# Optimization experiments

Hardware: AMD Instinct MI355X
Metric: run time of the kernel (lower is better)

## Reference

```python
import jax, jax.numpy as jnp
import numpy as np

CUTOFF = 5.0           # module init kwarg
NSYS, NAT = 64, 1000   # 64 systems of 1000 atoms each
BOX = 21.544           # cubic box edge -> ~0.1 atoms/A^3 (water-like density)
MAX_PAIRS = 2_200_000


def setup_inputs() -> dict:
    key = jax.random.key(0)
    coords = jax.random.uniform(key, (NSYS * NAT, 3), dtype=jnp.float32) * BOX
    isys = jnp.repeat(jnp.arange(NSYS, dtype=jnp.int32), NAT)
    natoms = jnp.full((NSYS,), NAT, dtype=jnp.int32)
    return {"coordinates": coords, "isys": isys, "natoms": natoms}


def reference(coordinates, isys, natoms):
    # Fixed-capacity cutoff neighbor list (no PBC branch), faithful to
    # GraphGeneratorFixed: half-list (i<j, same system), squared distances d12,
    # compacted into a MAX_PAIRS buffer padded with padding_value=N, then
    # symmetrized by concatenation.
    nsys = natoms.shape[0]
    n = coordinates.shape[0]
    nat = n // nsys                      # equal-sized systems (static)
    padding_value = n
    cutoff2 = jnp.float32(CUTOFF * CUTOFF)

    x = coordinates.reshape(nsys, nat, 3)                 # [S, nat, 3]
    sq = jnp.sum(x * x, axis=-1)                          # [S, nat]
    gram = jnp.einsum('sid,sjd->sij', x, x)               # [S, nat, nat]
    d12 = sq[:, :, None] + sq[:, None, :] - 2.0 * gram    # squared distances

    triu = jnp.triu(jnp.ones((nat, nat), dtype=bool), k=1)  # i < j half-list
    mask = (d12 < cutoff2) & triu[None, :, :]             # [S, nat, nat]
    mflat = mask.reshape(-1)                              # [S*nat*nat]
    npairs = jnp.sum(mflat)

    # stream-compaction: position of each kept pair in the output buffer
    pos = jnp.cumsum(mflat.astype(jnp.int32)) - 1
    sel = jnp.where(mflat, pos, MAX_PAIRS)                # OOB -> dropped
    flat_idx = jnp.arange(nsys * nat * nat, dtype=jnp.int32)
    idx_buf = jnp.full((MAX_PAIRS,), -1, dtype=jnp.int32).at[sel].set(
        flat_idx, mode='drop')

    valid = idx_buf >= 0
    ib = jnp.maximum(idx_buf, 0)
    s = ib // (nat * nat)
    rem = ib % (nat * nat)
    i = rem // nat
    j = rem % nat
    src = jnp.where(valid, s * nat + i, padding_value)
    dst = jnp.where(valid, s * nat + j, padding_value)
    d12_sel = jnp.where(valid, d12.reshape(-1)[ib], cutoff2)

    # symmetrize (directed graph), as in the original
    edge_src = jnp.concatenate([src, dst])
    edge_dst = jnp.concatenate([dst, src])
    d12_out = jnp.concatenate([d12_sel, d12_sel])
    return edge_src, edge_dst, d12_out, npairs
```

## Files before the change

kernel.cpp:

```cpp
#include <hip/hip_runtime.h>

#define NSYS 64
#define NAT  1000
#define NTOT (NSYS * NAT)
#define MP   2200000
#define CUT2 25.0f
#define PADV 64000.0f
#define SCAN_BLOCKS 250
#define CAP  104
#define EB   512
#define LCN  1152

__device__ __forceinline__ float dist2f(float xi, float yi, float zi,
                                        float xj, float yj, float zj) {
    float dx = xi - xj, dy = yi - yj, dz = zi - zj;
    return fmaf(dz, dz, fmaf(dy, dy, dx * dx));
}

__global__ __launch_bounds__(1024) void k_eval(const float* __restrict__ coords,
                                               int* __restrict__ counts,
                                               uint2* __restrict__ qbuf) {
    __shared__ float4 lc[LCN];
    int s      = blockIdx.x >> 3;
    int stripe = blockIdx.x & 7;
    const float* cs = coords + s * (NAT * 3);
    for (int a = threadIdx.x; a < NAT; a += 1024)
        lc[a] = make_float4(cs[3 * a], cs[3 * a + 1], cs[3 * a + 2], 0.0f);
    __syncthreads();
    int w    = threadIdx.x >> 6;
    int lane = threadIdx.x & 63;
    int W    = stripe * 16 + w;
    unsigned long long lt = (1ull << lane) - 1ull;
    for (int r = W; r < NAT; r += 128) {
        float4 ci = lc[r];
        int grow = s * NAT + r;
        uint2* q = qbuf + (size_t)grow * CAP;
        int running = 0;
        for (int jb = r + 1; jb < NAT; jb += 128) {
            int j  = jb + lane;
            int j2 = j + 64;
            float4 c0 = lc[j];
            float4 c1 = lc[j2];
            float d0 = dist2f(ci.x, ci.y, ci.z, c0.x, c0.y, c0.z);
            float d1 = dist2f(ci.x, ci.y, ci.z, c1.x, c1.y, c1.z);
            bool k0 = (j  < NAT) && (d0 < CUT2);
            bool k1 = (j2 < NAT) && (d1 < CUT2);
            unsigned long long m0 = __ballot(k0);
            unsigned long long m1 = __ballot(k1);
            if (k0) {
                int rank = running + (int)__popcll(m0 & lt);
                if (rank < CAP)
                    q[rank] = make_uint2((unsigned)(j - r), __float_as_uint(d0));
            }
            int base1 = running + (int)__popcll(m0);
            if (k1) {
                int rank = base1 + (int)__popcll(m1 & lt);
                if (rank < CAP)
                    q[rank] = make_uint2((unsigned)(j2 - r), __float_as_uint(d1));
            }
            running = base1 + (int)__popcll(m1);
        }
        if (lane == 0) counts[grow] = running;
    }
}

__global__ void k_scan_a(const int* __restrict__ counts, int* __restrict__ offs,
                         int* __restrict__ bsum) {
    __shared__ int tmp[256];
    int t = threadIdx.x;
    int g = blockIdx.x * 256 + t;
    int v = counts[g];
    tmp[t] = v;
    __syncthreads();
    for (int off = 1; off < 256; off <<= 1) {
        int u = (t >= off) ? tmp[t - off] : 0;
        __syncthreads();
        tmp[t] += u;
        __syncthreads();
    }
    offs[g] = tmp[t] - v;
    if (t == 255) bsum[blockIdx.x] = tmp[255];
}

__global__ __launch_bounds__(1024) void k_emitpad(const int* __restrict__ counts,
                                                  const int* __restrict__ offs,
                                                  const int* __restrict__ bsum,
                                                  const uint2* __restrict__ qbuf,
                                                  float* __restrict__ out) {
    __shared__ int bpre[256];
    __shared__ int stot;
    int t = threadIdx.x;
    int v = 0;
    if (t < 256) {
        v = (t < SCAN_BLOCKS) ? bsum[t] : 0;
        bpre[t] = v;
    }
    __syncthreads();
    for (int off = 1; off < 256; off <<= 1) {
        int u = 0;
        if (t < 256 && t >= off) u = bpre[t - off];
        __syncthreads();
        if (t < 256) bpre[t] += u;
        __syncthreads();
    }
    int incl = (t < 256) ? bpre[t] : 0;
    __syncthreads();
    if (t < 256) bpre[t] = incl - v;
    if (t == 255) stot = incl;
    __syncthreads();

    int wv   = t >> 6;
    int lane = t & 63;
    int GW   = blockIdx.x * 16 + wv;
    for (int r = GW; r < NTOT; r += EB * 16) {
        int off = offs[r] + bpre[r >> 8];
        int cnt = counts[r];
        if (cnt > CAP) cnt = CAP;
        const uint2* q = qbuf + (size_t)r * CAP;
        float fs = (float)r;
        for (int l = lane; l < cnt; l += 64) {
            uint2 e = q[l];
            int pos = off + l;
            if (pos < MP) {
                float fd = (float)(r + (int)e.x);
                float d2 = __uint_as_float(e.y);
                out[pos]          = fs;
                out[MP + pos]     = fd;
                out[2 * MP + pos] = fd;
                out[3 * MP + pos] = fs;
                out[4 * MP + pos] = d2;
                out[5 * MP + pos] = d2;
            }
        }
    }

    int total = stot;
    if (blockIdx.x == 0 && t == 0) out[6 * MP] = (float)total;
    int valid = total < MP ? total : MP;
    const int NQ = MP / 4;
    for (int q4 = blockIdx.x * 1024 + t; q4 < NQ; q4 += EB * 1024) {
        int k4 = q4 * 4;
        if (k4 + 4 <= valid) continue;
        if (k4 >= valid) {
            float4 vp = {PADV, PADV, PADV, PADV};
            float4 vc = {CUT2, CUT2, CUT2, CUT2};
            *(float4*)(out + k4)          = vp;
            *(float4*)(out + MP + k4)     = vp;
            *(float4*)(out + 2 * MP + k4) = vp;
            *(float4*)(out + 3 * MP + k4) = vp;
            *(float4*)(out + 4 * MP + k4) = vc;
            *(float4*)(out + 5 * MP + k4) = vc;
        } else {
#pragma unroll
            for (int e = 0; e < 4; e++) {
                int k = k4 + e;
                if (k >= valid && k < MP) {
                    out[k]          = PADV;
                    out[MP + k]     = PADV;
                    out[2 * MP + k] = PADV;
                    out[3 * MP + k] = PADV;
                    out[4 * MP + k] = CUT2;
                    out[5 * MP + k] = CUT2;
                }
            }
        }
    }
}

extern "C" void kernel_launch(void* const* d_in, const int* in_sizes, int n_in,
                              void* d_out, int out_size, void* d_ws, size_t ws_size,
                              hipStream_t stream) {
    const float* coords = (const float*)d_in[0];
    float* out = (float*)d_out;

    int*   counts = (int*)d_ws;
    int*   offs   = counts + NTOT;
    int*   bsum   = offs + NTOT;
    uint2* qbuf   = (uint2*)(bsum + 256);

    k_eval<<<EB, 1024, 0, stream>>>(coords, counts, qbuf);
    k_scan_a<<<SCAN_BLOCKS, 256, 0, stream>>>(counts, offs, bsum);
    k_emitpad<<<EB, 1024, 0, stream>>>(counts, offs, bsum, qbuf, out);
}
```

Before: 113.4 us.

## Make emit output-position-centric with binary search; zigzag row balancing in eval

The emit kernel is reorganised so each thread owns four consecutive output slots. A block-level binary search over the row prefix offsets, followed by a shared-memory search per thread, finds the source row for each slot. Every output column is then written with one coalesced float4 store that covers valid pairs and padding alike, replacing the row-major scattered scalar writes plus a separate padding pass. In the eval kernel, rows are assigned to waves in zigzag order to even out the triangular workload, and shared coordinates are padded with far-away sentinels so the main loop can drop bounds checks. The lane rank also switches to mbcnt. The cost is the extra search work per block and per thread, plus a dependence on no 4096-position tile spanning more than 512 rows.

```diff
diff --git a/kernel.cpp b/kernel.cpp
--- a/kernel.cpp
+++ b/kernel.cpp
@@ -10,11 +10,18 @@
 #define CAP  104
 #define EB   512
 #define LCN  1152
+#define NROWS 512
+#define POSB  4096
 
 __device__ __forceinline__ float dist2f(float xi, float yi, float zi,
                                         float xj, float yj, float zj) {
     float dx = xi - xj, dy = yi - yj, dz = zi - zj;
     return fmaf(dz, dz, fmaf(dy, dy, dx * dx));
+}
+
+__device__ __forceinline__ int mbcnt(unsigned long long m) {
+    unsigned lo = __builtin_amdgcn_mbcnt_lo((unsigned)m, 0u);
+    return (int)__builtin_amdgcn_mbcnt_hi((unsigned)(m >> 32), lo);
 }
 
 __global__ __launch_bounds__(1024) void k_eval(const float* __restrict__ coords,
@@ -24,19 +31,46 @@
     int s      = blockIdx.x >> 3;
     int stripe = blockIdx.x & 7;
     const float* cs = coords + s * (NAT * 3);
-    for (int a = threadIdx.x; a < NAT; a += 1024)
-        lc[a] = make_float4(cs[3 * a], cs[3 * a + 1], cs[3 * a + 2], 0.0f);
+    for (int a = threadIdx.x; a < LCN; a += 1024)
+        lc[a] = (a < NAT)
+              ? make_float4(cs[3 * a], cs[3 * a + 1], cs[3 * a + 2], 0.0f)
+              : make_float4(1.0e30f, 1.0e30f, 1.0e30f, 0.0f);
     __syncthreads();
     int w    = threadIdx.x >> 6;
     int lane = threadIdx.x & 63;
     int W    = stripe * 16 + w;
-    unsigned long long lt = (1ull << lane) - 1ull;
-    for (int r = W; r < NAT; r += 128) {
+    for (int t = 0;; t++) {
+        int r = ((t & 1) ? (127 - W) : W) + (t << 7);
+        if (r >= NAT) { if (((t & 1) ? W : (127 - W)) + (t << 7) >= NAT) break; else continue; }
         float4 ci = lc[r];
         int grow = s * NAT + r;
         uint2* q = qbuf + (size_t)grow * CAP;
         int running = 0;
-        for (int jb = r + 1; jb < NAT; jb += 128) {
+        int jb = r + 1;
+        for (; jb + 127 < NAT; jb += 128) {
+            int j  = jb + lane;
+            float4 c0 = lc[j];
+            float4 c1 = lc[j + 64];
+            float d0 = dist2f(ci.x, ci.y, ci.z, c0.x, c0.y, c0.z);
+            float d1 = dist2f(ci.x, ci.y, ci.z, c1.x, c1.y, c1.z);
+            bool k0 = d0 < CUT2;
+            bool k1 = d1 < CUT2;
+            unsigned long long m0 = __ballot(k0);
+            unsigned long long m1 = __ballot(k1);
+            if (k0) {
+                int rank = running + mbcnt(m0);
+                if (rank < CAP)
+                    q[rank] = make_uint2((unsigned)(j - r), __float_as_uint(d0));
+            }
+            int base1 = running + (int)__popcll(m0);
+            if (k1) {
+                int rank = base1 + mbcnt(m1);
+                if (rank < CAP)
+                    q[rank] = make_uint2((unsigned)(j + 64 - r), __float_as_uint(d1));
+            }
+            running = base1 + (int)__popcll(m1);
+        }
+        if (jb < NAT) {
             int j  = jb + lane;
             int j2 = j + 64;
             float4 c0 = lc[j];
@@ -48,13 +82,13 @@
             unsigned long long m0 = __ballot(k0);
             unsigned long long m1 = __ballot(k1);
             if (k0) {
-                int rank = running + (int)__popcll(m0 & lt);
+                int rank = running + mbcnt(m0);
                 if (rank < CAP)
                     q[rank] = make_uint2((unsigned)(j - r), __float_as_uint(d0));
             }
             int base1 = running + (int)__popcll(m0);
             if (k1) {
-                int rank = base1 + (int)__popcll(m1 & lt);
+                int rank = base1 + mbcnt(m1);
                 if (rank < CAP)
                     q[rank] = make_uint2((unsigned)(j2 - r), __float_as_uint(d1));
             }
@@ -82,13 +116,13 @@
     if (t == 255) bsum[blockIdx.x] = tmp[255];
 }
 
-__global__ __launch_bounds__(1024) void k_emitpad(const int* __restrict__ counts,
-                                                  const int* __restrict__ offs,
-                                                  const int* __restrict__ bsum,
-                                                  const uint2* __restrict__ qbuf,
-                                                  float* __restrict__ out) {
+__global__ __launch_bounds__(1024) void k_emit(const int* __restrict__ offs,
+                                               const int* __restrict__ bsum,
+                                               const uint2* __restrict__ qbuf,
+                                               float* __restrict__ out) {
     __shared__ int bpre[256];
-    __shared__ int stot;
+    __shared__ int lgoff[NROWS + 1];
+    __shared__ int sh_r0, sh_tot;
     int t = threadIdx.x;
     int v = 0;
     if (t < 256) {
@@ -106,62 +140,76 @@
     int incl = (t < 256) ? bpre[t] : 0;
     __syncthreads();
     if (t < 256) bpre[t] = incl - v;
-    if (t == 255) stot = incl;
-    __syncthreads();
-
-    int wv   = t >> 6;
-    int lane = t & 63;
-    int GW   = blockIdx.x * 16 + wv;
-    for (int r = GW; r < NTOT; r += EB * 16) {
-        int off = offs[r] + bpre[r >> 8];
-        int cnt = counts[r];
-        if (cnt > CAP) cnt = CAP;
-        const uint2* q = qbuf + (size_t)r * CAP;
-        float fs = (float)r;
-        for (int l = lane; l < cnt; l += 64) {
-            uint2 e = q[l];
-            int pos = off + l;
-            if (pos < MP) {
-                float fd = (float)(r + (int)e.x);
-                float d2 = __uint_as_float(e.y);
-                out[pos]          = fs;
-                out[MP + pos]     = fd;
-                out[2 * MP + pos] = fd;
-                out[3 * MP + pos] = fs;
-                out[4 * MP + pos] = d2;
-                out[5 * MP + pos] = d2;
-            }
-        }
-    }
-
-    int total = stot;
+    if (t == 255) sh_tot = incl;
+    __syncthreads();
+    int total = sh_tot;
+
+    int p0 = blockIdx.x * POSB;
+    if (t == 0) {
+        int lo = 0, hi = NTOT;
+        while (lo < hi) {
+            int mid = (lo + hi + 1) >> 1;
+            int g = (mid < NTOT) ? offs[mid] + bpre[mid >> 8] : total;
+            if (g <= p0) lo = mid; else hi = mid - 1;
+        }
+        sh_r0 = lo;
+    }
+    __syncthreads();
+    int r0 = sh_r0;
+    if (t <= NROWS) {
+        int r = r0 + t;
+        lgoff[t] = (r < NTOT) ? offs[r] + bpre[r >> 8] : total;
+    }
+    __syncthreads();
+
     if (blockIdx.x == 0 && t == 0) out[6 * MP] = (float)total;
     int valid = total < MP ? total : MP;
-    const int NQ = MP / 4;
-    for (int q4 = blockIdx.x * 1024 + t; q4 < NQ; q4 += EB * 1024) {
-        int k4 = q4 * 4;
-        if (k4 + 4 <= valid) continue;
-        if (k4 >= valid) {
-            float4 vp = {PADV, PADV, PADV, PADV};
-            float4 vc = {CUT2, CUT2, CUT2, CUT2};
-            *(float4*)(out + k4)          = vp;
-            *(float4*)(out + MP + k4)     = vp;
-            *(float4*)(out + 2 * MP + k4) = vp;
-            *(float4*)(out + 3 * MP + k4) = vp;
-            *(float4*)(out + 4 * MP + k4) = vc;
-            *(float4*)(out + 5 * MP + k4) = vc;
+
+    int p4 = p0 + t * 4;
+    if (p4 >= MP) return;
+    int k = 0;
+    for (int step = 256; step; step >>= 1) {
+        int nk = k + step;
+        if (nk <= NROWS - 1 && lgoff[nk] <= p4) k = nk;
+    }
+    float fs[4], fd[4], dd[4];
+#pragma unroll
+    for (int e = 0; e < 4; e++) {
+        int p = p4 + e;
+        if (p < valid) {
+            while (k < NROWS - 1 && lgoff[k + 1] <= p) k++;
+            int row = r0 + k;
+            int local = p - lgoff[k];
+            if (local > CAP - 1) local = CAP - 1;
+            uint2 rec = qbuf[(size_t)row * CAP + local];
+            fs[e] = (float)row;
+            fd[e] = (float)(row + (int)rec.x);
+            dd[e] = __uint_as_float(rec.y);
         } else {
+            fs[e] = PADV; fd[e] = PADV; dd[e] = CUT2;
+        }
+    }
+    if (p4 + 4 <= MP) {
+        float4 vs = {fs[0], fs[1], fs[2], fs[3]};
+        float4 vd = {fd[0], fd[1], fd[2], fd[3]};
+        float4 vv = {dd[0], dd[1], dd[2], dd[3]};
+        *(float4*)(out + p4)          = vs;
+        *(float4*)(out + MP + p4)     = vd;
+        *(float4*)(out + 2 * MP + p4) = vd;
+        *(float4*)(out + 3 * MP + p4) = vs;
+        *(float4*)(out + 4 * MP + p4) = vv;
+        *(float4*)(out + 5 * MP + p4) = vv;
+    } else {
 #pragma unroll
-            for (int e = 0; e < 4; e++) {
-                int k = k4 + e;
-                if (k >= valid && k < MP) {
-                    out[k]          = PADV;
-                    out[MP + k]     = PADV;
-                    out[2 * MP + k] = PADV;
-                    out[3 * MP + k] = PADV;
-                    out[4 * MP + k] = CUT2;
-                    out[5 * MP + k] = CUT2;
-                }
+        for (int e = 0; e < 4; e++) {
+            int p = p4 + e;
+            if (p < MP) {
+                out[p]          = fs[e];
+                out[MP + p]     = fd[e];
+                out[2 * MP + p] = fd[e];
+                out[3 * MP + p] = fs[e];
+                out[4 * MP + p] = dd[e];
+                out[5 * MP + p] = dd[e];
             }
         }
     }
@@ -178,7 +226,8 @@
     int*   bsum   = offs + NTOT;
     uint2* qbuf   = (uint2*)(bsum + 256);
 
+    int emit_blocks = (MP + POSB - 1) / POSB;
     k_eval<<<EB, 1024, 0, stream>>>(coords, counts, qbuf);
     k_scan_a<<<SCAN_BLOCKS, 256, 0, stream>>>(counts, offs, bsum);
-    k_emitpad<<<EB, 1024, 0, stream>>>(counts, offs, bsum, qbuf, out);
-}
+    k_emit<<<emit_blocks, 1024, 0, stream>>>(offs, bsum, qbuf, out);
+}
```

Result: no change. 113.1 us (-0.3%).
